# Optimization experiments

Hardware: AMD Instinct MI355X
Metric: run time of the kernel (lower is better)

## Reference

```python
import jax, jax.numpy as jnp
import numpy as np

B, LQ, LIM = 4, 640, 1296
D_MODEL, NHEAD, DFF, MAX_DIST = 768, 12, 3072, 100
DK = D_MODEL // NHEAD
EPS = 1e-5


def _layer_norm(x, g, b):
    mu = jnp.mean(x, axis=-1, keepdims=True)
    var = jnp.mean(jnp.square(x - mu), axis=-1, keepdims=True)
    return (x - mu) * jax.lax.rsqrt(var + EPS) * g + b


def setup_inputs() -> dict:
    key = jax.random.key(0)
    ks = jax.random.split(key, 24)
    s = 0.02
    inp = {
        "docqa": jax.random.normal(ks[0], (B, LQ, D_MODEL), jnp.float32),
        "im_tokens": jax.random.normal(ks[1], (B, LIM, D_MODEL), jnp.float32),
        "docqa_x": jax.random.randint(ks[2], (B, LQ), 0, 1000, jnp.int32),
        "docqa_y": jax.random.randint(ks[3], (B, LQ), 0, 1000, jnp.int32),
        "im_tokens_x": jax.random.randint(ks[4], (B, LIM), 0, 1000, jnp.int32),
        "im_tokens_y": jax.random.randint(ks[5], (B, LIM), 0, 1000, jnp.int32),
        # attention projection params
        "Wq": jax.random.normal(ks[6], (D_MODEL, D_MODEL), jnp.float32) * s,
        "bq": jnp.zeros((D_MODEL,), jnp.float32),
        "Wk": jax.random.normal(ks[7], (D_MODEL, D_MODEL), jnp.float32) * s,
        "bk": jnp.zeros((D_MODEL,), jnp.float32),
        "Wv": jax.random.normal(ks[8], (D_MODEL, D_MODEL), jnp.float32) * s,
        "bv": jnp.zeros((D_MODEL,), jnp.float32),
        "Wo": jax.random.normal(ks[9], (D_MODEL, D_MODEL), jnp.float32) * s,
        "bo": jnp.zeros((D_MODEL,), jnp.float32),
        # relative position bias tables: (2*max_dist+1, nhead) per axis
        "bias_x": jax.random.normal(ks[10], (2 * MAX_DIST + 1, NHEAD), jnp.float32) * s,
        "bias_y": jax.random.normal(ks[11], (2 * MAX_DIST + 1, NHEAD), jnp.float32) * s,
        # FFN
        "W1": jax.random.normal(ks[12], (D_MODEL, DFF), jnp.float32) * s,
        "b1": jnp.zeros((DFF,), jnp.float32),
        "W2": jax.random.normal(ks[13], (DFF, D_MODEL), jnp.float32) * s,
        "b2": jnp.zeros((D_MODEL,), jnp.float32),
        # LayerNorms
        "g1": jnp.ones((D_MODEL,), jnp.float32),
        "be1": jnp.zeros((D_MODEL,), jnp.float32),
        "g2": jnp.ones((D_MODEL,), jnp.float32),
        "be2": jnp.zeros((D_MODEL,), jnp.float32),
    }
    return inp


def reference(docqa, im_tokens, docqa_x, docqa_y, im_tokens_x, im_tokens_y,
              Wq, bq, Wk, bk, Wv, bv, Wo, bo, bias_x, bias_y,
              W1, b1, W2, b2, g1, be1, g2, be2):
    # keys/values attend over concatenated image tokens + docqa tokens
    full = jnp.concatenate([im_tokens, docqa], axis=1)            # (B, Lk, D)
    full_x = jnp.concatenate([im_tokens_x, docqa_x], axis=1)      # (B, Lk)
    full_y = jnp.concatenate([im_tokens_y, docqa_y], axis=1)

    q = (docqa @ Wq + bq).reshape(B, LQ, NHEAD, DK)               # (B,Lq,H,Dk)
    k = (full @ Wk + bk).reshape(B, LQ + LIM, NHEAD, DK)
    v = (full @ Wv + bv).reshape(B, LQ + LIM, NHEAD, DK)

    scores = jnp.einsum("bqhd,bkhd->bhqk", q, k) / jnp.sqrt(jnp.float32(DK))

    # relative-position bias, clamped to [-max_dist, max_dist]
    rel_x = jnp.clip(docqa_x[:, :, None] - full_x[:, None, :], -MAX_DIST, MAX_DIST) + MAX_DIST
    rel_y = jnp.clip(docqa_y[:, :, None] - full_y[:, None, :], -MAX_DIST, MAX_DIST) + MAX_DIST
    pos_bias = bias_x[rel_x] + bias_y[rel_y]                      # (B,Lq,Lk,H)
    scores = scores + jnp.transpose(pos_bias, (0, 3, 1, 2))       # (B,H,Lq,Lk)

    attn = jax.nn.softmax(scores, axis=-1)
    ctx = jnp.einsum("bhqk,bkhd->bqhd", attn, v).reshape(B, LQ, D_MODEL)
    attn_out = ctx @ Wo + bo

    # residual + norm + FFN + residual + norm (dropout=0 in eval)
    src = _layer_norm(docqa + attn_out, g1, be1)
    ffn = jnp.maximum(src @ W1 + b1, 0.0) @ W2 + b2
    src = _layer_norm(src + ffn, g2, be2)
    return src
```

## Files before the change

### kernel.cpp

```cpp
#include <hip/hip_runtime.h>
#include <hip/hip_bf16.h>

constexpr int B      = 4;
constexpr int LQ     = 640;
constexpr int LIM    = 1296;
constexpr int LK     = LQ + LIM;
constexpr int DM     = 768;
constexpr int NHEAD  = 12;
constexpr int DK     = 64;
constexpr int DFF    = 3072;
constexpr int MAXD   = 100;
constexpr int M_DOC  = B * LQ;
constexpr int M_FULL = B * LK;
constexpr size_t ML_CNT = (size_t)B * NHEAD * LQ;
constexpr int NPREP  = M_FULL * (DM / 8) / 256;

typedef __attribute__((ext_vector_type(8))) short bf16x8_t;
typedef __attribute__((ext_vector_type(4))) float f32x4_t;

__device__ __forceinline__ float b2f(__hip_bfloat16 x) { return __bfloat162float(x); }

__device__ __forceinline__ float ldf(const void* p, size_t i, int f32flag) {
    return f32flag ? ((const float*)p)[i]
                   : b2f(((const __hip_bfloat16*)p)[i]);
}

__device__ __forceinline__ void gl_lds16(const void* g, void* l) {
    __builtin_amdgcn_global_load_lds(
        (const __attribute__((address_space(1))) unsigned int*)g,
        (__attribute__((address_space(3))) unsigned int*)l, 16, 0, 0);
}

__device__ __forceinline__ void wtrans_tile(const void* W, __hip_bfloat16* Wt,
                                            int f32, int K, int N, int n0, int k0,
                                            __hip_bfloat16 (*t)[33])
{
    const int tx = threadIdx.x & 31, ty = threadIdx.x >> 5;
#pragma unroll
    for (int j = 0; j < 4; ++j) {
        int k = ty + j * 8;
        t[k][tx] = __float2bfloat16(ldf(W, (size_t)(k0 + k) * N + n0 + tx, f32));
    }
    __syncthreads();
#pragma unroll
    for (int j = 0; j < 4; ++j) {
        int n = ty + j * 8;
        Wt[(size_t)(n0 + n) * K + k0 + tx] = t[tx][n];
    }
}

__global__ __launch_bounds__(256)
void prep_wt3_kernel(const void* __restrict__ g1, int* __restrict__ flagp,
                     const void* __restrict__ im, const void* __restrict__ docqa,
                     const int* __restrict__ dqx, const int* __restrict__ dqy,
                     const int* __restrict__ imx, const int* __restrict__ imy,
                     const void* __restrict__ Wq, const void* __restrict__ Wk,
                     const void* __restrict__ Wv,
                     __hip_bfloat16* __restrict__ fullA,
                     int* __restrict__ cxy,
                     __hip_bfloat16* __restrict__ Wt3)
{
    __shared__ __hip_bfloat16 t[32][33];
    const bool f32 = ((*(const unsigned*)g1) & 0xFFFFu) == 0u;
    const int bx = blockIdx.x;

    if (bx >= NPREP) {
        const int id  = bx - NPREP;
        const int wid = id / 576;
        const int tt  = id % 576;
        const void* W = (wid == 0) ? Wq : (wid == 1) ? Wk : Wv;
        wtrans_tile(W, Wt3 + (size_t)wid * DM * DM, f32 ? 1 : 0, DM, DM,
                    (tt % 24) * 32, (tt / 24) * 32, t);
        return;
    }

    if (bx == 0 && threadIdx.x == 0) *flagp = f32 ? 1 : 0;

    const int gid = bx * 256 + threadIdx.x;
    if (gid < B * LK) {
        int b = gid / LK, l = gid - b * LK;
        const int x = (l < LIM) ? imx[b * LIM + l] : dqx[b * LQ + l - LIM];
        const int y = (l < LIM) ? imy[b * LIM + l] : dqy[b * LQ + l - LIM];
        cxy[gid] = (x & 0xFFFF) | (y << 16);
    }

    const int row = gid / (DM / 8);
    const int col = (gid - row * (DM / 8)) * 8;
    const int b   = row / LK;
    const int l   = row - b * LK;
    const size_t srow = (l < LIM) ? ((size_t)(b * LIM + l)) * DM
                                  : ((size_t)(b * LQ + (l - LIM))) * DM;
    const void* src = (l < LIM) ? im : docqa;
    union { bf16x8_t v; __hip_bfloat16 h[8]; } pk;
    if (f32) {
        const float4* fp = (const float4*)((const float*)src + srow + col);
        float4 a = fp[0], c = fp[1];
        pk.h[0] = __float2bfloat16(a.x); pk.h[1] = __float2bfloat16(a.y);
        pk.h[2] = __float2bfloat16(a.z); pk.h[3] = __float2bfloat16(a.w);
        pk.h[4] = __float2bfloat16(c.x); pk.h[5] = __float2bfloat16(c.y);
        pk.h[6] = __float2bfloat16(c.z); pk.h[7] = __float2bfloat16(c.w);
    } else {
        pk.v = *(const bf16x8_t*)((const __hip_bfloat16*)src + srow + col);
    }
    *(bf16x8_t*)(fullA + (size_t)row * DM + col) = pk.v;
}

__global__ __launch_bounds__(256)
void qkv_gemm(const __hip_bfloat16* __restrict__ fullA,
              const __hip_bfloat16* __restrict__ Wt3,
              const void* __restrict__ bq,
              const void* __restrict__ bk,
              const void* __restrict__ bv,
              __hip_bfloat16* __restrict__ qout,
              __hip_bfloat16* __restrict__ kb,
              __hip_bfloat16* __restrict__ vtb,
              const int* __restrict__ flagp)
{
    __shared__ __hip_bfloat16 Als[128 * 32];
    __shared__ __hip_bfloat16 Bls[128 * 32];

    const int f32  = *flagp;
    const int tid  = threadIdx.x;
    const int lane = tid & 63;
    const int wave = tid >> 6;
    const int quad = lane >> 4;
    const int c16  = lane & 15;

    const int id = blockIdx.x;
    int n0, m0;
    if (id < 732) {
        n0 = DM + (id % 12) * 128;
        m0 = (id / 12) * 128;
    } else {
        const int t = id - 732;
        n0 = (t % 6) * 128;
        m0 = (t / 6) * 128;
    }
    const int seg = n0 / DM;

    const int wm   = (wave >> 1) * 64;
    const int wn   = (wave & 1) * 64;
    constexpr int K = DM;

    f32x4_t acc[4][4] = {};

    for (int k0 = 0; k0 < K; k0 += 32) {
#pragma unroll
        for (int p = 0; p < 2; ++p) {
            const int lin = p * 64 + lane;
            int row = wave * 32 + (lin >> 2);
            int gr  = m0 + row;
            if (seg == 0) {
                const int bb = gr / LQ;
                gr = bb * LK + LIM + (gr - bb * LQ);
            } else if (gr > M_FULL - 1) gr = M_FULL - 1;
            gl_lds16(fullA + (size_t)gr * K + k0 + (lin & 3) * 8,
                     Als + wave * 1024 + p * 512);
        }
#pragma unroll
        for (int p = 0; p < 2; ++p) {
            const int lin = p * 64 + lane;
            const int row = wave * 32 + (lin >> 2);
            gl_lds16(Wt3 + (size_t)(n0 + row) * K + k0 + (lin & 3) * 8,
                     Bls + wave * 1024 + p * 512);
        }
        __syncthreads();

        bf16x8_t af[4], bfr[4];
#pragma unroll
        for (int i = 0; i < 4; ++i)
            af[i] = *(const bf16x8_t*)(Als + (wm + i * 16 + c16) * 32 + quad * 8);
#pragma unroll
        for (int j = 0; j < 4; ++j)
            bfr[j] = *(const bf16x8_t*)(Bls + (wn + j * 16 + c16) * 32 + quad * 8);
#pragma unroll
        for (int i = 0; i < 4; ++i)
#pragma unroll
            for (int j = 0; j < 4; ++j)
                acc[i][j] = __builtin_amdgcn_mfma_f32_16x16x32_bf16(af[i], bfr[j], acc[i][j], 0, 0, 0);
        __syncthreads();
    }

    const void* bptr = (seg == 0) ? bq : (seg == 1) ? bk : bv;
#pragma unroll
    for (int j = 0; j < 4; ++j) {
        const int col  = n0 + wn + j * 16 + c16;
        const int ncol = col - seg * DM;
        const float bj = ldf(bptr, ncol, f32);
        if (seg == 2) {
            const int h = ncol >> 6, d = ncol & 63;
#pragma unroll
            for (int i = 0; i < 4; ++i) {
                const int rowb = m0 + wm + i * 16 + quad * 4;
                const int bb0  = rowb / LK;
                const int l0   = rowb - bb0 * LK;
                if (l0 + 3 < LK && rowb + 3 < M_FULL) {
                    union { ushort4 u4; __hip_bfloat16 hh[4]; } pk;
#pragma unroll
                    for (int r = 0; r < 4; ++r)
                        pk.hh[r] = __float2bfloat16(acc[i][j][r] + bj);
                    *(ushort4*)(vtb + ((size_t)((bb0 * NHEAD + h) * DK + d)) * LK + l0) = pk.u4;
                } else {
#pragma unroll
                    for (int r = 0; r < 4; ++r) {
                        const int row = rowb + r;
                        if (row < M_FULL) {
                            int bb = row / LK, l = row - bb * LK;
                            vtb[((size_t)((bb * NHEAD + h) * DK + d)) * LK + l] =
                                __float2bfloat16(acc[i][j][r] + bj);
                        }
                    }
                }
            }
        } else if (seg == 1) {
#pragma unroll
            for (int i = 0; i < 4; ++i) {
                const int rowb = m0 + wm + i * 16 + quad * 4;
#pragma unroll
                for (int r = 0; r < 4; ++r) {
                    const int row = rowb + r;
                    if (row < M_FULL)
                        kb[(size_t)row * DM + ncol] = __float2bfloat16(acc[i][j][r] + bj);
                }
            }
        } else {
#pragma unroll
            for (int i = 0; i < 4; ++i) {
                const int rowb = m0 + wm + i * 16 + quad * 4;
#pragma unroll
                for (int r = 0; r < 4; ++r)
                    qout[(size_t)(rowb + r) * DM + ncol] =
                        __float2bfloat16((acc[i][j][r] + bj) * 0.125f);
            }
        }
    }
}

__global__ __launch_bounds__(256)
void mfma_gemm_relu(const __hip_bfloat16* __restrict__ Abf,
                    const __hip_bfloat16* __restrict__ Wt,
                    const void* __restrict__ bias,
                    __hip_bfloat16* __restrict__ Cc,
                    const int* __restrict__ flagp,
                    int M, int N, int K)
{
    __shared__ __hip_bfloat16 Als[128 * 32];
    __shared__ __hip_bfloat16 Bls[128 * 32];

    const int f32  = *flagp;
    const int tid  = threadIdx.x;
    const int lane = tid & 63;
    const int wave = tid >> 6;
    const int quad = lane >> 4;
    const int c16  = lane & 15;
    const int n0   = blockIdx.x * 128;
    const int m0   = blockIdx.y * 128;
    const int wm   = (wave >> 1) * 64;
    const int wn   = (wave & 1) * 64;

    f32x4_t acc[4][4] = {};

    for (int k0 = 0; k0 < K; k0 += 32) {
#pragma unroll
        for (int p = 0; p < 2; ++p) {
            const int lin = p * 64 + lane;
            int row = wave * 32 + (lin >> 2);
            int gr  = m0 + row; if (gr > M - 1) gr = M - 1;
            gl_lds16(Abf + (size_t)gr * K + k0 + (lin & 3) * 8, Als + wave * 1024 + p * 512);
        }
#pragma unroll
        for (int p = 0; p < 2; ++p) {
            const int lin = p * 64 + lane;
            const int row = wave * 32 + (lin >> 2);
            gl_lds16(Wt + (size_t)(n0 + row) * K + k0 + (lin & 3) * 8,
                     Bls + wave * 1024 + p * 512);
        }
        __syncthreads();

        bf16x8_t af[4], bfr[4];
#pragma unroll
        for (int i = 0; i < 4; ++i)
            af[i] = *(const bf16x8_t*)(Als + (wm + i * 16 + c16) * 32 + quad * 8);
#pragma unroll
        for (int j = 0; j < 4; ++j)
            bfr[j] = *(const bf16x8_t*)(Bls + (wn + j * 16 + c16) * 32 + quad * 8);
#pragma unroll
        for (int i = 0; i < 4; ++i)
#pragma unroll
            for (int j = 0; j < 4; ++j)
                acc[i][j] = __builtin_amdgcn_mfma_f32_16x16x32_bf16(af[i], bfr[j], acc[i][j], 0, 0, 0);
        __syncthreads();
    }

#pragma unroll
    for (int j = 0; j < 4; ++j) {
        const int col = n0 + wn + j * 16 + c16;
        const float bj = ldf(bias, col, f32);
#pragma unroll
        for (int i = 0; i < 4; ++i) {
            const int rowb = m0 + wm + i * 16 + quad * 4;
#pragma unroll
            for (int r = 0; r < 4; ++r) {
                const int row = rowb + r;
                if (row < M) {
                    float v = fmaxf(acc[i][j][r] + bj, 0.f);
                    Cc[(size_t)row * N + col] = __float2bfloat16(v);
                }
            }
        }
    }
}

__global__ __launch_bounds__(256)
void sk_gemm(const __hip_bfloat16* __restrict__ Abf,
             const __hip_bfloat16* __restrict__ Wt,
             float* __restrict__ Cc,
             int M, int N, int K, int S)
{
    __shared__ __hip_bfloat16 Als[128 * 32];
    __shared__ __hip_bfloat16 Bls[128 * 32];

    const int tid  = threadIdx.x;
    const int lane = tid & 63;
    const int wave = tid >> 6;
    const int quad = lane >> 4;
    const int c16  = lane & 15;
    const int n0   = blockIdx.x * 128;
    const int m0   = blockIdx.y * 128;
    const int wm   = (wave >> 1) * 64;
    const int wn   = (wave & 1) * 64;
    const int kchunk = K / S;
    const int kbeg = blockIdx.z * kchunk;

    f32x4_t acc[4][4] = {};

    for (int k0 = kbeg; k0 < kbeg + kchunk; k0 += 32) {
#pragma unroll
        for (int p = 0; p < 2; ++p) {
            const int lin = p * 64 + lane;
            int row = wave * 32 + (lin >> 2);
            int gr  = m0 + row; if (gr > M - 1) gr = M - 1;
            gl_lds16(Abf + (size_t)gr * K + k0 + (lin & 3) * 8, Als + wave * 1024 + p * 512);
        }
#pragma unroll
        for (int p = 0; p < 2; ++p) {
            const int lin = p * 64 + lane;
            const int row = wave * 32 + (lin >> 2);
            gl_lds16(Wt + (size_t)(n0 + row) * K + k0 + (lin & 3) * 8,
                     Bls + wave * 1024 + p * 512);
        }
        __syncthreads();

        bf16x8_t af[4], bfr[4];
#pragma unroll
        for (int i = 0; i < 4; ++i)
            af[i] = *(const bf16x8_t*)(Als + (wm + i * 16 + c16) * 32 + quad * 8);
#pragma unroll
        for (int j = 0; j < 4; ++j)
            bfr[j] = *(const bf16x8_t*)(Bls + (wn + j * 16 + c16) * 32 + quad * 8);
#pragma unroll
        for (int i = 0; i < 4; ++i)
#pragma unroll
            for (int j = 0; j < 4; ++j)
                acc[i][j] = __builtin_amdgcn_mfma_f32_16x16x32_bf16(af[i], bfr[j], acc[i][j], 0, 0, 0);
        __syncthreads();
    }

#pragma unroll
    for (int j = 0; j < 4; ++j) {
        const int col = n0 + wn + j * 16 + c16;
#pragma unroll
        for (int i = 0; i < 4; ++i) {
            const int rowb = m0 + wm + i * 16 + quad * 4;
#pragma unroll
            for (int r = 0; r < 4; ++r) {
                const int row = rowb + r;
                if (row < M) atomicAdd(&Cc[(size_t)row * N + col], acc[i][j][r]);
            }
        }
    }
}

__global__ __launch_bounds__(256)
void attn_part_kernel(const __hip_bfloat16* __restrict__ Qb,
                      const __hip_bfloat16* __restrict__ Kb,
                      const __hip_bfloat16* __restrict__ Vtb,
                      const int* __restrict__ cxy,
                      const void* __restrict__ bias_x,
                      const void* __restrict__ bias_y,
                      __hip_bfloat16* __restrict__ p0,
                      __hip_bfloat16* __restrict__ p1,
                      float* __restrict__ mlbase,
                      const int* __restrict__ flagp)
{
    constexpr int QT = 64, KT = 64;
    constexpr int QROW = 72;
    __shared__ __hip_bfloat16 Qs[QT * DK];
    __shared__ __hip_bfloat16 Ks[KT * DK];
    __shared__ __hip_bfloat16 Vs[DK * KT];
    __shared__ __hip_bfloat16 Ps[QT * QROW];
    __shared__ float bxs[2 * MAXD + 1], bys[2 * MAXD + 1];

    const int f32  = *flagp;
    const int tid  = threadIdx.x;
    const int lane = tid & 63;
    const int wave = tid >> 6;
    const int quad = lane >> 4;
    const int c16  = lane & 15;

    const int id   = blockIdx.x;
    const int bh   = id % 48;
    const int rest = id / 48;
    const int s    = rest & 1;
    const int q0   = (rest >> 1) * QT;
    const int b    = bh / NHEAD;
    const int h    = bh - b * NHEAD;
    const int kbeg = s * 1024;
    const int kend = s ? LK : 1024;

    __hip_bfloat16* Op = s ? p1 : p0;
    float* mp = mlbase + (size_t)s * 2 * ML_CNT;
    float* lp = mp + ML_CNT;

    for (int i = tid; i < 2 * MAXD + 1; i += 256) {
        bxs[i] = ldf(bias_x, (size_t)i * NHEAD + h, f32);
        bys[i] = ldf(bias_y, (size_t)i * NHEAD + h, f32);
    }

    const __hip_bfloat16* kbase = Kb + ((size_t)(b * LK)) * DM + h * DK;
    const __hip_bfloat16* vbase = Vtb + ((size_t)((b * NHEAD + h) * DK)) * LK;
    const __hip_bfloat16* qbase = Qb + ((size_t)(b * LQ + q0)) * DM + h * DK;
    const int* cb_ = cxy + b * LK;

    {
        const int rsub0 = lane >> 3;
        const int cg0   = (lane & 7) ^ (rsub0 & 7);
#pragma unroll
        for (int p = 0; p < 2; ++p) {
            const int rl = wave * 16 + p * 8 + rsub0;
            gl_lds16(qbase + (size_t)rl * DM + cg0 * 8, Qs + (wave * 16 + p * 8) * DK);
        }
    }

    int qxp[4], qyp[4];
#pragma unroll
    for (int r = 0; r < 4; ++r) {
        const int v = cb_[LIM + q0 + wave * 16 + quad * 4 + r];
        qxp[r] = (v & 0xFFFF) + MAXD;
        qyp[r] = (v >> 16) + MAXD;
    }

    __syncthreads();

    const int sw  = c16 & 7;
    const int cA0 = (quad ^ sw) * 8;
    const int cA1 = ((quad + 4) ^ sw) * 8;
    const int rQ  = wave * 16 + c16;
    const bf16x8_t aq0 = *(const bf16x8_t*)(Qs + rQ * DK + cA0);
    const bf16x8_t aq1 = *(const bf16x8_t*)(Qs + rQ * DK + cA1);

    f32x4_t O[4] = {};
    float m_r[4], l_r[4];
#pragma unroll
    for (int r = 0; r < 4; ++r) { m_r[r] = -1e30f; l_r[r] = 0.f; }

    const int rsub = lane >> 3;
    const int cgl  = (lane & 7) ^ (rsub & 7);

    for (int k0 = kbeg; k0 < kend; k0 += KT) {
#pragma unroll
        for (int p = 0; p < 2; ++p) {
            const int rl = wave * 16 + p * 8 + rsub;
            int gr = k0 + rl; if (gr > LK - 1) gr = LK - 1;
            gl_lds16(kbase + (size_t)gr * DM + cgl * 8, Ks + (wave * 16 + p * 8) * DK);
        }
#pragma unroll
        for (int p = 0; p < 2; ++p) {
            const int dl = wave * 16 + p * 8 + rsub;
            int kks = k0 + cgl * 8; if (kks > LK - 8) kks = LK - 8;
            gl_lds16(vbase + (size_t)dl * LK + kks, Vs + (wave * 16 + p * 8) * KT);
        }
        __syncthreads();

        f32x4_t S[4];
#pragma unroll
        for (int jn = 0; jn < 4; ++jn) {
            const int rK = jn * 16 + c16;
            bf16x8_t bk0 = *(const bf16x8_t*)(Ks + rK * DK + cA0);
            bf16x8_t bk1 = *(const bf16x8_t*)(Ks + rK * DK + cA1);
            f32x4_t acc = {0.f, 0.f, 0.f, 0.f};
            acc = __builtin_amdgcn_mfma_f32_16x16x32_bf16(aq0, bk0, acc, 0, 0, 0);
            acc = __builtin_amdgcn_mfma_f32_16x16x32_bf16(aq1, bk1, acc, 0, 0, 0);
            S[jn] = acc;
        }
#pragma unroll
        for (int jn = 0; jn < 4; ++jn) {
            const int kg = k0 + jn * 16 + c16;
            const bool ok = kg < LK;
            const int kv = cb_[ok ? kg : LK - 1];
            const int kx = kv & 0xFFFF, ky = kv >> 16;
#pragma unroll
            for (int r = 0; r < 4; ++r) {
                int rx = min(max(qxp[r] - kx, 0), 2 * MAXD);
                int ry = min(max(qyp[r] - ky, 0), 2 * MAXD);
                float v = S[jn][r] + bxs[rx] + bys[ry];
                S[jn][r] = ok ? v : -1e30f;
            }
        }
        float alpha[4];
#pragma unroll
        for (int r = 0; r < 4; ++r) {
            float mx = fmaxf(fmaxf(S[0][r], S[1][r]), fmaxf(S[2][r], S[3][r]));
            mx = fmaxf(mx, __shfl_xor(mx, 1));
            mx = fmaxf(mx, __shfl_xor(mx, 2));
            mx = fmaxf(mx, __shfl_xor(mx, 4));
            mx = fmaxf(mx, __shfl_xor(mx, 8));
            const float mt = fmaxf(m_r[r], mx);
            const float al = __expf(m_r[r] - mt);
            float sum = 0.f;
#pragma unroll
            for (int jn = 0; jn < 4; ++jn) {
                float p = __expf(S[jn][r] - mt);
                S[jn][r] = p;
                sum += p;
            }
            m_r[r] = mt;
            l_r[r] = l_r[r] * al + sum;
            alpha[r] = al;
        }
#pragma unroll
        for (int jn = 0; jn < 4; ++jn)
#pragma unroll
            for (int r = 0; r < 4; ++r)
                Ps[(wave * 16 + quad * 4 + r) * QROW + jn * 16 + c16] = __float2bfloat16(S[jn][r]);
#pragma unroll
        for (int jd = 0; jd < 4; ++jd)
#pragma unroll
            for (int r = 0; r < 4; ++r) O[jd][r] *= alpha[r];
        bf16x8_t ap0 = *(const bf16x8_t*)(Ps + (wave * 16 + c16) * QROW + quad * 8);
        bf16x8_t ap1 = *(const bf16x8_t*)(Ps + (wave * 16 + c16) * QROW + 32 + quad * 8);
#pragma unroll
        for (int jd = 0; jd < 4; ++jd) {
            const int rV = jd * 16 + c16;
            bf16x8_t bv0 = *(const bf16x8_t*)(Vs + rV * KT + cA0);
            bf16x8_t bv1 = *(const bf16x8_t*)(Vs + rV * KT + cA1);
            O[jd] = __builtin_amdgcn_mfma_f32_16x16x32_bf16(ap0, bv0, O[jd], 0, 0, 0);
            O[jd] = __builtin_amdgcn_mfma_f32_16x16x32_bf16(ap1, bv1, O[jd], 0, 0, 0);
        }
        __syncthreads();
    }

#pragma unroll
    for (int r = 0; r < 4; ++r) {
        float ls = l_r[r];
        ls += __shfl_xor(ls, 1);
        ls += __shfl_xor(ls, 2);
        ls += __shfl_xor(ls, 4);
        ls += __shfl_xor(ls, 8);
        const int ql = wave * 16 + quad * 4 + r;
        const size_t grow = (size_t)(b * LQ + q0 + ql);
#pragma unroll
        for (int jd = 0; jd < 4; ++jd)
            Op[grow * DM + h * DK + jd * 16 + c16] = __float2bfloat16(O[jd][r]);
        if (c16 == 0) {
            size_t mli = ((size_t)b * NHEAD + h) * LQ + q0 + ql;
            mp[mli] = m_r[r];
            lp[mli] = ls;
        }
    }
}

__global__ __launch_bounds__(256)
void merge_wt_kernel(const __hip_bfloat16* __restrict__ p0,
                     const __hip_bfloat16* __restrict__ p1,
                     const float* __restrict__ mlbase,
                     __hip_bfloat16* __restrict__ ctx,
                     float* __restrict__ aof,
                     const void* __restrict__ Wo,
                     __hip_bfloat16* __restrict__ WtO,
                     const void* __restrict__ W1,
                     const void* __restrict__ W2,
                     __hip_bfloat16* __restrict__ W1t,
                     __hip_bfloat16* __restrict__ W2t,
                     const int* __restrict__ flagp)
{
    __shared__ __hip_bfloat16 t[32][33];
    const int bx = blockIdx.x;

    if (bx >= M_DOC + 576) {
        const int id = bx - (M_DOC + 576);
        const int f32 = *flagp;
        const bool second = id >= 2304;
        const void* W = second ? W2 : W1;
        __hip_bfloat16* dst = second ? W2t : W1t;
        const int K = second ? DFF : DM;
        const int N = second ? DM : DFF;
        const int tt = second ? id - 2304 : id;
        const int nt = N / 32;
        wtrans_tile(W, dst, f32, K, N, (tt % nt) * 32, (tt / nt) * 32, t);
        return;
    }
    if (bx >= M_DOC) {
        const int tt = bx - M_DOC;
        wtrans_tile(Wo, WtO, *flagp, DM, DM, (tt % 24) * 32, (tt / 24) * 32, t);
        return;
    }

    const int row = bx;
    const int b = row / LQ, q = row - b * LQ;
    const int tid = threadIdx.x;
#pragma unroll
    for (int i = 0; i < 3; ++i) {
        const int c = tid + i * 256;
        const int h = c >> 6;
        const size_t mli = ((size_t)b * NHEAD + h) * LQ + q;
        const float m0 = mlbase[mli],              l0 = mlbase[ML_CNT + mli];
        const float m1 = mlbase[2 * ML_CNT + mli], l1 = mlbase[3 * ML_CNT + mli];
        const float mm = fmaxf(m0, m1);
        const float w0 = __expf(m0 - mm), w1 = __expf(m1 - mm);
        const float denom = l0 * w0 + l1 * w1;
        const size_t idx = (size_t)row * DM + c;
        const float v = (b2f(p0[idx]) * w0 + b2f(p1[idx]) * w1) / denom;
        ctx[idx] = __float2bfloat16(v);
        aof[idx] = 0.f;
    }
}

template<int MODE>
__global__ __launch_bounds__(256)
void ln_kernel(const void* __restrict__ Xin,
               const __hip_bfloat16* __restrict__ Xb,
               const float* __restrict__ Xf2f,
               const void* __restrict__ bias2,
               const void* __restrict__ g,
               const void* __restrict__ be,
               __hip_bfloat16* __restrict__ outb,
               void* __restrict__ outv,
               float* __restrict__ zbuf,
               const int* __restrict__ flagp)
{
    __shared__ float red1[4], red2[4];
    const int f32 = *flagp;
    const int row = blockIdx.x;
    const int tid = threadIdx.x;
    const int lane = tid & 63;
    const int wave = tid >> 6;

    float x[3];
#pragma unroll
    for (int i = 0; i < 3; ++i) {
        int c = tid + i * 256;
        size_t idx = (size_t)row * DM + c;
        float a  = (MODE == 0) ? ldf(Xin, idx, f32) : b2f(Xb[idx]);
        x[i] = a + Xf2f[idx] + ldf(bias2, c, f32);
    }
    float s1 = x[0] + x[1] + x[2];
    float s2 = x[0] * x[0] + x[1] * x[1] + x[2] * x[2];
#pragma unroll
    for (int off = 32; off > 0; off >>= 1) {
        s1 += __shfl_xor(s1, off);
        s2 += __shfl_xor(s2, off);
    }
    if (lane == 0) { red1[wave] = s1; red2[wave] = s2; }
    __syncthreads();
    s1 = red1[0] + red1[1] + red1[2] + red1[3];
    s2 = red2[0] + red2[1] + red2[2] + red2[3];
    float mu   = s1 * (1.f / DM);
    float var  = s2 * (1.f / DM) - mu * mu;
    float rstd = rsqrtf(var + 1e-5f);
#pragma unroll
    for (int i = 0; i < 3; ++i) {
        int c = tid + i * 256;
        size_t idx = (size_t)row * DM + c;
        float v = (x[i] - mu) * rstd * ldf(g, c, f32) + ldf(be, c, f32);
        if (MODE == 0) {
            outb[idx] = __float2bfloat16(v);
            zbuf[idx] = 0.f;
        } else {
            if (f32) ((float*)outv)[idx] = v;
            else     ((__hip_bfloat16*)outv)[idx] = __float2bfloat16(v);
        }
    }
}

extern "C" void kernel_launch(void* const* d_in, const int* in_sizes, int n_in,
                              void* d_out, int out_size, void* d_ws, size_t ws_size,
                              hipStream_t stream)
{
    const void* docqa = d_in[0];
    const void* im    = d_in[1];
    const int* dqx = (const int*)d_in[2];
    const int* dqy = (const int*)d_in[3];
    const int* imx = (const int*)d_in[4];
    const int* imy = (const int*)d_in[5];
    const void* Wq = d_in[6];
    const void* bq = d_in[7];
    const void* Wk = d_in[8];
    const void* bk = d_in[9];
    const void* Wv = d_in[10];
    const void* bv = d_in[11];
    const void* Wo = d_in[12];
    const void* bo = d_in[13];
    const void* bias_x = d_in[14];
    const void* bias_y = d_in[15];
    const void* W1 = d_in[16];
    const void* b1 = d_in[17];
    const void* W2 = d_in[18];
    const void* b2 = d_in[19];
    const void* g1  = d_in[20];
    const void* be1 = d_in[21];
    const void* g2  = d_in[22];
    const void* be2 = d_in[23];

    char* w = (char*)d_ws;
    int*            flagp = (int*)w;
    __hip_bfloat16* qR  = (__hip_bfloat16*)(w + 256);
    __hip_bfloat16* kb  = qR + (size_t)M_DOC  * DM;
    __hip_bfloat16* vtb = kb + (size_t)M_FULL * DM;
    __hip_bfloat16* cb  = vtb + (size_t)M_FULL * DM;
    char* cbB = (char*)cb;
    char* r1B = (char*)qR;

    __hip_bfloat16* fullA = cb;
    __hip_bfloat16* Wt3  = qR;
    int*            cxyp = (int*)(r1B + 3538944);
    __hip_bfloat16* WtO  = qR;
    __hip_bfloat16* qout = (__hip_bfloat16*)d_out;
    __hip_bfloat16* p0   = cb;
    __hip_bfloat16* p1   = (__hip_bfloat16*)(cbB + 3932160);
    float*          mlb  = (float*)(cbB + 7864320);
    __hip_bfloat16* ctx  = cb;
    __hip_bfloat16* src1 = cb;
    float*          fof  = (float*)(cbB + 3932160);
    float*          aof  = (float*)kb;
    __hip_bfloat16* W1t  = vtb;
    __hip_bfloat16* W2t  = vtb + (size_t)DFF * DM;
    __hip_bfloat16* mid  = qR;

    dim3 blk(256);

    prep_wt3_kernel<<<dim3(NPREP + 3 * 576), blk, 0, stream>>>(
        g1, flagp, im, docqa, dqx, dqy, imx, imy, Wq, Wk, Wv, fullA, cxyp, Wt3);
    qkv_gemm<<<dim3(732 + 120), blk, 0, stream>>>(
        fullA, Wt3, bq, bk, bv, qout, kb, vtb, flagp);
    attn_part_kernel<<<dim3(48 * 20), blk, 0, stream>>>(
        qout, kb, vtb, cxyp, bias_x, bias_y, p0, p1, mlb, flagp);
    merge_wt_kernel<<<dim3(M_DOC + 576 + 4608), blk, 0, stream>>>(
        p0, p1, mlb, ctx, aof, Wo, WtO, W1, W2, W1t, W2t, flagp);
    sk_gemm<<<dim3(DM / 128, M_DOC / 128, 4), blk, 0, stream>>>(
        ctx, WtO, aof, M_DOC, DM, DM, 4);
    ln_kernel<0><<<dim3(M_DOC), blk, 0, stream>>>(
        docqa, nullptr, aof, bo, g1, be1, src1, nullptr, fof, flagp);
    mfma_gemm_relu<<<dim3(DFF / 128, M_DOC / 128), blk, 0, stream>>>(
        src1, W1t, b1, mid, flagp, M_DOC, DFF, DM);
    sk_gemm<<<dim3(DM / 128, M_DOC / 128, 4), blk, 0, stream>>>(
        mid, W2t, fof, M_DOC, DM, DFF, 4);
    ln_kernel<1><<<dim3(M_DOC), blk, 0, stream>>>(
        nullptr, src1, fof, b2, g2, be2, nullptr, d_out, nullptr, flagp);
}
```

Measured before the change: 379.5 us.

## Split attention keys three ways and alias Q/P shared memory to raise occupancy

Splits the key range of the attention kernel into three chunks instead of two, which launches more blocks (1440 instead of 960) and gives each block a shorter loop. The merge kernel now combines three partial outputs using their max and sum statistics. Shared memory use per block drops: the Q tile and the P buffer share one allocation, with a barrier added after Q is loaded into registers, and the bias tables are stored as bf16. This should allow more resident blocks, but it adds partial-output traffic and merge work, and rounds the bias to bf16.

```diff
diff --git a/kernel.cpp b/kernel.cpp
--- a/kernel.cpp
+++ b/kernel.cpp
@@ -14,6 +14,7 @@
 constexpr int M_FULL = B * LK;
 constexpr size_t ML_CNT = (size_t)B * NHEAD * LQ;
 constexpr int NPREP  = M_FULL * (DM / 8) / 256;
+constexpr int NSPLIT = 3;
 
 typedef __attribute__((ext_vector_type(8))) short bf16x8_t;
 typedef __attribute__((ext_vector_type(4))) float f32x4_t;
@@ -388,18 +389,18 @@
                       const int* __restrict__ cxy,
                       const void* __restrict__ bias_x,
                       const void* __restrict__ bias_y,
-                      __hip_bfloat16* __restrict__ p0,
-                      __hip_bfloat16* __restrict__ p1,
+                      __hip_bfloat16* __restrict__ pparts,
                       float* __restrict__ mlbase,
                       const int* __restrict__ flagp)
 {
     constexpr int QT = 64, KT = 64;
     constexpr int QROW = 72;
-    __shared__ __hip_bfloat16 Qs[QT * DK];
+    __shared__ char PQraw[QT * QROW * 2];
     __shared__ __hip_bfloat16 Ks[KT * DK];
     __shared__ __hip_bfloat16 Vs[DK * KT];
-    __shared__ __hip_bfloat16 Ps[QT * QROW];
-    __shared__ float bxs[2 * MAXD + 1], bys[2 * MAXD + 1];
+    __shared__ __hip_bfloat16 bxs[2 * MAXD + 1], bys[2 * MAXD + 1];
+    __hip_bfloat16* Qs = (__hip_bfloat16*)PQraw;
+    __hip_bfloat16* Ps = (__hip_bfloat16*)PQraw;
 
     const int f32  = *flagp;
     const int tid  = threadIdx.x;
@@ -411,20 +412,20 @@
     const int id   = blockIdx.x;
     const int bh   = id % 48;
     const int rest = id / 48;
-    const int s    = rest & 1;
-    const int q0   = (rest >> 1) * QT;
+    const int s    = rest % NSPLIT;
+    const int q0   = (rest / NSPLIT) * QT;
     const int b    = bh / NHEAD;
     const int h    = bh - b * NHEAD;
-    const int kbeg = s * 1024;
-    const int kend = s ? LK : 1024;
-
-    __hip_bfloat16* Op = s ? p1 : p0;
+    const int kbeg = s * 640;
+    const int kend = (s == NSPLIT - 1) ? LK : kbeg + 640;
+
+    __hip_bfloat16* Op = pparts + (size_t)s * M_DOC * DM;
     float* mp = mlbase + (size_t)s * 2 * ML_CNT;
     float* lp = mp + ML_CNT;
 
     for (int i = tid; i < 2 * MAXD + 1; i += 256) {
-        bxs[i] = ldf(bias_x, (size_t)i * NHEAD + h, f32);
-        bys[i] = ldf(bias_y, (size_t)i * NHEAD + h, f32);
+        bxs[i] = __float2bfloat16(ldf(bias_x, (size_t)i * NHEAD + h, f32));
+        bys[i] = __float2bfloat16(ldf(bias_y, (size_t)i * NHEAD + h, f32));
     }
 
     const __hip_bfloat16* kbase = Kb + ((size_t)(b * LK)) * DM + h * DK;
@@ -458,6 +459,8 @@
     const int rQ  = wave * 16 + c16;
     const bf16x8_t aq0 = *(const bf16x8_t*)(Qs + rQ * DK + cA0);
     const bf16x8_t aq1 = *(const bf16x8_t*)(Qs + rQ * DK + cA1);
+    asm volatile("s_waitcnt lgkmcnt(0)" ::: "memory");
+    __syncthreads();
 
     f32x4_t O[4] = {};
     float m_r[4], l_r[4];
@@ -503,7 +506,7 @@
             for (int r = 0; r < 4; ++r) {
                 int rx = min(max(qxp[r] - kx, 0), 2 * MAXD);
                 int ry = min(max(qyp[r] - ky, 0), 2 * MAXD);
-                float v = S[jn][r] + bxs[rx] + bys[ry];
+                float v = S[jn][r] + b2f(bxs[rx]) + b2f(bys[ry]);
                 S[jn][r] = ok ? v : -1e30f;
             }
         }
@@ -571,8 +574,7 @@
 }
 
 __global__ __launch_bounds__(256)
-void merge_wt_kernel(const __hip_bfloat16* __restrict__ p0,
-                     const __hip_bfloat16* __restrict__ p1,
+void merge_wt_kernel(const __hip_bfloat16* __restrict__ pparts,
                      const float* __restrict__ mlbase,
                      __hip_bfloat16* __restrict__ ctx,
                      float* __restrict__ aof,
@@ -614,13 +616,16 @@
         const int c = tid + i * 256;
         const int h = c >> 6;
         const size_t mli = ((size_t)b * NHEAD + h) * LQ + q;
-        const float m0 = mlbase[mli],              l0 = mlbase[ML_CNT + mli];
-        const float m1 = mlbase[2 * ML_CNT + mli], l1 = mlbase[3 * ML_CNT + mli];
-        const float mm = fmaxf(m0, m1);
-        const float w0 = __expf(m0 - mm), w1 = __expf(m1 - mm);
-        const float denom = l0 * w0 + l1 * w1;
+        const float m0 = mlbase[mli],                  l0 = mlbase[ML_CNT + mli];
+        const float m1 = mlbase[2 * ML_CNT + mli],     l1 = mlbase[3 * ML_CNT + mli];
+        const float m2 = mlbase[4 * ML_CNT + mli],     l2 = mlbase[5 * ML_CNT + mli];
+        const float mm = fmaxf(m0, fmaxf(m1, m2));
+        const float w0 = __expf(m0 - mm), w1 = __expf(m1 - mm), w2 = __expf(m2 - mm);
+        const float denom = l0 * w0 + l1 * w1 + l2 * w2;
         const size_t idx = (size_t)row * DM + c;
-        const float v = (b2f(p0[idx]) * w0 + b2f(p1[idx]) * w1) / denom;
+        const float v = (b2f(pparts[idx]) * w0 +
+                         b2f(pparts[(size_t)M_DOC * DM + idx]) * w1 +
+                         b2f(pparts[(size_t)2 * M_DOC * DM + idx]) * w2) / denom;
         ctx[idx] = __float2bfloat16(v);
         aof[idx] = 0.f;
     }
@@ -726,9 +731,8 @@
     int*            cxyp = (int*)(r1B + 3538944);
     __hip_bfloat16* WtO  = qR;
     __hip_bfloat16* qout = (__hip_bfloat16*)d_out;
-    __hip_bfloat16* p0   = cb;
-    __hip_bfloat16* p1   = (__hip_bfloat16*)(cbB + 3932160);
-    float*          mlb  = (float*)(cbB + 7864320);
+    __hip_bfloat16* pparts = cb;
+    float*          mlb  = (float*)(r1B + 1179648);
     __hip_bfloat16* ctx  = cb;
     __hip_bfloat16* src1 = cb;
     float*          fof  = (float*)(cbB + 3932160);
@@ -743,10 +747,10 @@
         g1, flagp, im, docqa, dqx, dqy, imx, imy, Wq, Wk, Wv, fullA, cxyp, Wt3);
     qkv_gemm<<<dim3(732 + 120), blk, 0, stream>>>(
         fullA, Wt3, bq, bk, bv, qout, kb, vtb, flagp);
-    attn_part_kernel<<<dim3(48 * 20), blk, 0, stream>>>(
-        qout, kb, vtb, cxyp, bias_x, bias_y, p0, p1, mlb, flagp);
+    attn_part_kernel<<<dim3(48 * 30), blk, 0, stream>>>(
+        qout, kb, vtb, cxyp, bias_x, bias_y, pparts, mlb, flagp);
     merge_wt_kernel<<<dim3(M_DOC + 576 + 4608), blk, 0, stream>>>(
-        p0, p1, mlb, ctx, aof, Wo, WtO, W1, W2, W1t, W2t, flagp);
+        pparts, mlb, ctx, aof, Wo, WtO, W1, W2, W1t, W2t, flagp);
     sk_gemm<<<dim3(DM / 128, M_DOC / 128, 4), blk, 0, stream>>>(
         ctx, WtO, aof, M_DOC, DM, DM, 4);
     ln_kernel<0><<<dim3(M_DOC), blk, 0, stream>>>(
```

Measured after the change: 379.7 us. No clear change (+0.0%).
